# Performance work log

Hardware: AMD Instinct MI355X
Metric: run time of the kernel (lower is better)

The kernel has to match this reference:

```python
import jax, jax.numpy as jnp
import numpy as np

B, S, D, H, DFF = 4, 2048, 2048, 16, 8192
DH = D // H
THETA = 10000.0
EPS = 1e-5


def rmsnorm(x, g):
    return x * jax.lax.rsqrt(jnp.mean(x * x, axis=-1, keepdims=True) + EPS) * g


def rope(x, pos):
    # x: [B, H, S, DH]; rotate interleaved even/odd pairs
    half = DH // 2
    inv_freq = THETA ** (-(jnp.arange(half, dtype=jnp.float32) * 2.0) / DH)  # [half]
    ang = pos.astype(jnp.float32)[:, None] * inv_freq  # [S, half]
    cos, sin = jnp.cos(ang), jnp.sin(ang)
    x1, x2 = x[..., 0::2], x[..., 1::2]
    r1 = x1 * cos - x2 * sin
    r2 = x1 * sin + x2 * cos
    return jnp.stack([r1, r2], axis=-1).reshape(x.shape)


def setup_inputs() -> dict:
    key = jax.random.key(0)
    ks = jax.random.split(key, 12)
    s = 0.02
    return {
        "x": jax.random.normal(ks[0], (B, S, D), dtype=jnp.float32),
        "attention_mask": jnp.ones((S, S), dtype=bool),
        "wq": jax.random.normal(ks[1], (D, D), dtype=jnp.float32) * s,
        "wk": jax.random.normal(ks[2], (D, D), dtype=jnp.float32) * s,
        "wv": jax.random.normal(ks[3], (D, D), dtype=jnp.float32) * s,
        "wo": jax.random.normal(ks[4], (D, D), dtype=jnp.float32) * s,
        "w1": jax.random.normal(ks[5], (DFF, D), dtype=jnp.float32) * s,
        "w2": jax.random.normal(ks[6], (D, DFF), dtype=jnp.float32) * s,
        "w3": jax.random.normal(ks[7], (DFF, D), dtype=jnp.float32) * s,
        "g1": jnp.ones((D,), dtype=jnp.float32),
        "g2": jnp.ones((D,), dtype=jnp.float32),
    }


def reference(x, attention_mask, wq, wk, wv, wo, w1, w2, w3, g1, g2):
    pos = jnp.arange(x.shape[-2])
    # pre-norm attention
    h = rmsnorm(x, g1)
    q = (h @ wq.T).reshape(B, S, H, DH).transpose(0, 2, 1, 3)
    k = (h @ wk.T).reshape(B, S, H, DH).transpose(0, 2, 1, 3)
    v = (h @ wv.T).reshape(B, S, H, DH).transpose(0, 2, 1, 3)
    q = rope(q, pos)
    k = rope(k, pos)
    scores = jnp.einsum("bhqd,bhkd->bhqk", q, k) / np.float32(np.sqrt(DH))
    scores = jnp.where(attention_mask, scores, jnp.float32(-1e9))
    attn = jax.nn.softmax(scores, axis=-1)
    o = jnp.einsum("bhqk,bhkd->bhqd", attn, v)
    o = o.transpose(0, 2, 1, 3).reshape(B, S, D) @ wo.T
    x = x + o
    # pre-norm SwiGLU FFN
    h2 = rmsnorm(x, g2)
    ffn = (jax.nn.silu(h2 @ w1.T) * (h2 @ w3.T)) @ w2.T
    return x + ffn
```

## Files before the change

kernel.cpp:

```cpp
#include <hip/hip_runtime.h>
#include <cstdint>
#include <cstddef>

#define B_   4
#define S_   2048
#define D_   2048
#define H_   16
#define DH_  128
#define DFF_ 8192
#define LOG2E 1.4426950408889634f

typedef __bf16 bf16_t;
typedef __bf16 bf16x4 __attribute__((ext_vector_type(4)));
typedef __bf16 bf16x8 __attribute__((ext_vector_type(8)));
typedef float  f32x4  __attribute__((ext_vector_type(4)));

#define MFMA16 __builtin_amdgcn_mfma_f32_16x16x32_bf16

__device__ __forceinline__ void glds16(const void* g, void* l) {
  __builtin_amdgcn_global_load_lds((__attribute__((address_space(1))) void*)g,
                                   (__attribute__((address_space(3))) void*)l,
                                   16, 0, 0);
}

__global__ __launch_bounds__(256) void cvt_kernel(const float* __restrict__ in,
                                                  bf16_t* __restrict__ out, int n8) {
  int i = blockIdx.x * 256 + threadIdx.x;
  if (i >= n8) return;
  const float4* p4 = (const float4*)in;
  float4 a = p4[2 * (size_t)i];
  float4 b = p4[2 * (size_t)i + 1];
  bf16x8 o;
  o[0] = (bf16_t)a.x; o[1] = (bf16_t)a.y; o[2] = (bf16_t)a.z; o[3] = (bf16_t)a.w;
  o[4] = (bf16_t)b.x; o[5] = (bf16_t)b.y; o[6] = (bf16_t)b.z; o[7] = (bf16_t)b.w;
  ((bf16x8*)out)[i] = o;
}

__global__ __launch_bounds__(256) void rmsnorm_kernel(const float* __restrict__ x,
                                                      const float* __restrict__ g,
                                                      bf16_t* __restrict__ out) {
  const int row = blockIdx.x, tid = threadIdx.x;
  const float* xr = x + (size_t)row * D_;
  float4 a = ((const float4*)xr)[tid * 2];
  float4 b = ((const float4*)xr)[tid * 2 + 1];
  float ss = a.x*a.x + a.y*a.y + a.z*a.z + a.w*a.w
           + b.x*b.x + b.y*b.y + b.z*b.z + b.w*b.w;
#pragma unroll
  for (int m = 1; m < 64; m <<= 1) ss += __shfl_xor(ss, m);
  __shared__ float red[4];
  if ((tid & 63) == 0) red[tid >> 6] = ss;
  __syncthreads();
  float tot = red[0] + red[1] + red[2] + red[3];
  float rms = rsqrtf(tot * (1.0f / D_) + 1e-5f);
  float4 ga = ((const float4*)g)[tid * 2];
  float4 gb = ((const float4*)g)[tid * 2 + 1];
  bf16x8 o;
  o[0] = (bf16_t)(a.x * rms * ga.x); o[1] = (bf16_t)(a.y * rms * ga.y);
  o[2] = (bf16_t)(a.z * rms * ga.z); o[3] = (bf16_t)(a.w * rms * ga.w);
  o[4] = (bf16_t)(b.x * rms * gb.x); o[5] = (bf16_t)(b.y * rms * gb.y);
  o[6] = (bf16_t)(b.z * rms * gb.z); o[7] = (bf16_t)(b.w * rms * gb.w);
  ((bf16x8*)out)[(size_t)row * 256 + tid] = o;
}


#define RD_A_S(d, s)                                                          \
  do {                                                                        \
    const char* p_ = ldsb + (d) * 32768 + ((s) * 64 + l15) * 128;             \
    _Pragma("unroll") for (int i_ = 0; i_ < 4; i_++) {                        \
      afr[i_][0] = *(const bf16x8*)(p_ + i_ * 2048 + acol0);                  \
      afr[i_][1] = *(const bf16x8*)(p_ + i_ * 2048 + acol1);                  \
    }                                                                         \
  } while (0)

#define RD_B(d)                                                               \
  do {                                                                        \
    const char* p_ = ldsb + 65536 + (d) * 32768 + (wn * 32 + l15) * 128;      \
    _Pragma("unroll") for (int j_ = 0; j_ < 2; j_++) {                        \
      bfr[j_][0] = *(const bf16x8*)(p_ + j_ * 2048 + acol0);                  \
      bfr[j_][1] = *(const bf16x8*)(p_ + j_ * 2048 + acol1);                  \
    }                                                                         \
  } while (0)

#define STAGE_A_LO(d, kt)                                                     \
  do {                                                                        \
    char* dst_ = ldsb + (d) * 32768 + o0;                                     \
    const bf16_t* s_ = Asrc + (size_t)(kt) * 64;                              \
    glds16(s_, dst_);                                                         \
    glds16(s_ + 64 * (size_t)K, dst_ + 8192);                                 \
  } while (0)

#define STAGE_A_HI(d, kt)                                                     \
  do {                                                                        \
    char* dst_ = ldsb + (d) * 32768 + 16384 + o0;                             \
    const bf16_t* s_ = Asrc + (size_t)(kt) * 64 + 128 * (size_t)K;            \
    glds16(s_, dst_);                                                         \
    glds16(s_ + 64 * (size_t)K, dst_ + 8192);                                 \
  } while (0)

#define STAGE_B_LO(d, kt)                                                     \
  do {                                                                        \
    char* dst_ = ldsb + 65536 + (d) * 32768 + o0;                             \
    const bf16_t* s_ = Wsrc + (size_t)(kt) * 64;                              \
    glds16(s_, dst_);                                                         \
    glds16(s_ + 64 * (size_t)K, dst_ + 8192);                                 \
  } while (0)

#define STAGE_B_HI(d, kt)                                                     \
  do {                                                                        \
    char* dst_ = ldsb + 65536 + (d) * 32768 + 16384 + o0;                     \
    const bf16_t* s_ = Wsrc + (size_t)(kt) * 64 + 128 * (size_t)K;            \
    glds16(s_, dst_);                                                         \
    glds16(s_ + 64 * (size_t)K, dst_ + 8192);                                 \
  } while (0)

#define MFMA_S(s)                                                             \
  do {                                                                        \
    __builtin_amdgcn_s_setprio(1);                                            \
    _Pragma("unroll") for (int i_ = 0; i_ < 4; i_++)                          \
    _Pragma("unroll") for (int j_ = 0; j_ < 2; j_++) {                        \
      acc[(s)*4 + i_][j_] = MFMA16(afr[i_][0], bfr[j_][0], acc[(s)*4 + i_][j_], 0,0,0); \
      acc[(s)*4 + i_][j_] = MFMA16(afr[i_][1], bfr[j_][1], acc[(s)*4 + i_][j_], 0,0,0); \
    }                                                                         \
    __builtin_amdgcn_s_setprio(0);                                            \
  } while (0)

#define PHASE_FENCE()                                                         \
  do {                                                                        \
    __builtin_amdgcn_sched_barrier(0);                                        \
    __builtin_amdgcn_s_barrier();                                             \
  } while (0)

template <int EPI>
__global__ __launch_bounds__(512, 2) void gemm256(const bf16_t* __restrict__ A,
                                                  const bf16_t* __restrict__ W,
                                                  const float* __restrict__ addf,
                                                  const bf16_t* __restrict__ addb,
                                                  bf16_t* __restrict__ outb,
                                                  bf16_t* __restrict__ outb2,
                                                  bf16_t* __restrict__ outb3,
                                                  float* __restrict__ outf,
                                                  int M, int N, int K) {
  __shared__ char ldsb[131072];
  const int tid = threadIdx.x;
  const int wid = tid >> 6, l = tid & 63, l15 = l & 15, lg = l >> 4;
  const int wn = wid;

  const int nwg = gridDim.x;
  int wg = (int)blockIdx.x;
  wg = (wg & 7) * (nwg >> 3) + (wg >> 3);
  const int ntn = N >> 8;
  const int m0 = (wg / ntn) << 8, n0 = (wg % ntn) << 8;

  f32x4 acc[16][2];
  const f32x4 z4 = {0.f, 0.f, 0.f, 0.f};
#pragma unroll
  for (int i = 0; i < 16; i++) { acc[i][0] = z4; acc[i][1] = z4; }

  const int o0 = tid * 16;
  const int srow = o0 >> 7;
  const int ssw = ((o0 & 127) ^ ((srow & 7) << 4)) >> 1;
  const bf16_t* Asrc = A + (size_t)(m0 + srow) * K + ssw;
  const bf16_t* Wsrc = W + (size_t)(n0 + srow) * K + ssw;

  const int rsw = (l15 & 7) << 4;
  const int acol0 = (lg * 16) ^ rsw;
  const int acol1 = (64 + lg * 16) ^ rsw;

  bf16x8 afr[4][2], bfr[2][2];

  const int NT = K >> 6;
  STAGE_A_LO(0, 0); STAGE_A_HI(0, 0); STAGE_B_LO(0, 0); STAGE_B_HI(0, 0);
  STAGE_B_LO(1, 1); STAGE_A_LO(1, 1); STAGE_B_HI(1, 1);
  asm volatile("s_waitcnt vmcnt(6)" ::: "memory");
  __builtin_amdgcn_s_barrier();

  for (int t = 0; t < NT; t++) {
    const int d = t & 1;
    RD_B(d);
    RD_A_S(d, 0);
    if (t + 1 < NT) STAGE_A_HI(d ^ 1, t + 1);
    PHASE_FENCE();
    MFMA_S(0);
    PHASE_FENCE();
    RD_A_S(d, 1);
    if (t + 2 < NT) STAGE_B_LO(d, t + 2);
    PHASE_FENCE();
    MFMA_S(1);
    PHASE_FENCE();
    RD_A_S(d, 2);
    if (t + 2 < NT) STAGE_A_LO(d, t + 2);
    PHASE_FENCE();
    MFMA_S(2);
    PHASE_FENCE();
    RD_A_S(d, 3);
    if (t + 2 < NT) STAGE_B_HI(d, t + 2);
    PHASE_FENCE();
    MFMA_S(3);
    if (t + 2 < NT) asm volatile("s_waitcnt vmcnt(6)" ::: "memory");
    else            asm volatile("s_waitcnt vmcnt(0)" ::: "memory");
    __builtin_amdgcn_sched_barrier(0);
    __builtin_amdgcn_s_barrier();
  }

#pragma unroll
  for (int m = 0; m < 16; m++) {
    const int gr = m0 + m * 16 + lg * 4;
#pragma unroll
    for (int nn = 0; nn < 2; nn++) {
      const int gc = n0 + wn * 32 + nn * 16 + l15;
      if constexpr (EPI == 4) {
        const int seg = gc >> 11;
        const int gcl = gc & 2047;
        if (seg < 2) {
          bf16_t* o = seg ? outb2 : outb;
#pragma unroll
          for (int r = 0; r < 4; r++)
            o[(size_t)(gr + r) * D_ + gcl] = (bf16_t)acc[m][nn][r];
        } else {
          const int bb = gr >> 11, ss = gr & 2047;
          bf16x4 pk;
#pragma unroll
          for (int r = 0; r < 4; r++) pk[r] = (bf16_t)acc[m][nn][r];
          *(bf16x4*)(outb3 + ((size_t)bb * D_ + gcl) * S_ + ss) = pk;
        }
      } else {
#pragma unroll
        for (int r = 0; r < 4; r++) {
          size_t idx = (size_t)(gr + r) * N + gc;
          if constexpr (EPI == 0) {
            outb[idx] = (bf16_t)acc[m][nn][r];
          } else if constexpr (EPI == 1) {
            outf[idx] = acc[m][nn][r] + addf[idx];
          } else {
            float a1v = (float)addb[idx];
            outb[idx] = (bf16_t)(a1v / (1.0f + expf(-a1v)) * acc[m][nn][r]);
          }
        }
      }
    }
  }
}

__global__ __launch_bounds__(256) void rope_kernel(bf16_t* __restrict__ buf) {
  size_t i = (size_t)blockIdx.x * 256 + threadIdx.x;
  int pi = (int)(i & 63);
  size_t rh = i >> 6;
  int srow = (int)((rh / H_) % S_);
  float inv = expf((float)pi * (-9.210340371976184f / 64.0f));
  float ang = (float)srow * inv;
  float c = cosf(ang), sn = sinf(ang);
  bf16_t* p = buf + i * 2;
  float x1 = (float)p[0], x2 = (float)p[1];
  p[0] = (bf16_t)(x1 * c - x2 * sn);
  p[1] = (bf16_t)(x1 * sn + x2 * c);
}

__global__ __launch_bounds__(256) void attn_kernel(const bf16_t* __restrict__ Q,
                                                   const bf16_t* __restrict__ Kb,
                                                   const bf16_t* __restrict__ Vt,
                                                   bf16_t* __restrict__ O) {
  const int qt = blockIdx.x, h = blockIdx.y, b = blockIdx.z;
  const int tid = threadIdx.x;
  const int wid = tid >> 6, l = tid & 63, l15 = l & 15, lg = l >> 4;

  __shared__ bf16_t Klds[32 * 128];
  __shared__ bf16_t Vlds[128 * 32];
  __shared__ bf16_t Plds[4][16 * 40];

  const int q0 = qt * 64 + wid * 16;
  const f32x4 z4 = {0.f, 0.f, 0.f, 0.f};

  bf16x8 qf[4];
  {
    const bf16_t* qp = Q + ((size_t)(b * S_ + q0 + l15)) * D_ + h * DH_ + lg * 8;
#pragma unroll
    for (int kk = 0; kk < 4; kk++) qf[kk] = *(const bf16x8*)(qp + kk * 32);
  }
  f32x4 of[8];
#pragma unroll
  for (int f = 0; f < 8; f++) of[f] = z4;
  float m_run = -1e30f, l_run = 0.f;

  const int o0 = tid * 16;
  const int krow0 = o0 >> 8;
  const int kcolb = o0 & 255;
  const int scol = (kcolb ^ ((krow0 & 7) << 4)) >> 1;
  const int vrow0 = o0 >> 6;
  const int vc = (o0 >> 4) & 3;
  const int vcol = (vc ^ ((vrow0 >> 1) & 3)) << 3;
  const int vxor = (l15 >> 1) & 3;

  const size_t bh_off = ((size_t)b * S_) * D_ + (size_t)h * DH_;
  const bf16_t* vtbase = Vt + ((size_t)b * D_ + h * DH_) * S_;

  for (int kv0 = 0; kv0 < S_; kv0 += 32) {
    const bf16_t* kbase = Kb + bh_off + (size_t)kv0 * D_;
    glds16(kbase + (size_t)krow0 * D_ + scol,        (char*)Klds + wid * 1024);
    glds16(kbase + (size_t)(krow0 + 16) * D_ + scol, (char*)Klds + wid * 1024 + 4096);
    glds16(vtbase + (size_t)vrow0 * S_ + kv0 + vcol,        (char*)Vlds + wid * 1024);
    glds16(vtbase + (size_t)(vrow0 + 64) * S_ + kv0 + vcol, (char*)Vlds + wid * 1024 + 4096);
    __syncthreads();

    f32x4 st[2];
#pragma unroll
    for (int c = 0; c < 2; c++) {
      st[c] = z4;
      const int row = c * 16 + l15;
      const char* kr = (const char*)Klds + row * 256;
      const int sw = (row & 7) << 4;
#pragma unroll
      for (int kk = 0; kk < 4; kk++) {
        bf16x8 kf = *(const bf16x8*)(kr + ((kk * 64 + lg * 16) ^ sw));
        st[c] = MFMA16(kf, qf[kk], st[c], 0, 0, 0);
      }
    }

    float s[8];
#pragma unroll
    for (int c = 0; c < 2; c++)
#pragma unroll
      for (int r = 0; r < 4; r++) s[c * 4 + r] = st[c][r] * 0.08838834764831845f;
    float pm = s[0];
#pragma unroll
    for (int i = 1; i < 8; i++) pm = fmaxf(pm, s[i]);
    pm = fmaxf(pm, __shfl_xor(pm, 16));
    pm = fmaxf(pm, __shfl_xor(pm, 32));
    float mnew = fmaxf(m_run, pm);
    float alpha = exp2f((m_run - mnew) * LOG2E);
    float p[8], ts = 0.f;
#pragma unroll
    for (int i = 0; i < 8; i++) { p[i] = exp2f((s[i] - mnew) * LOG2E); ts += p[i]; }
    ts += __shfl_xor(ts, 16);
    ts += __shfl_xor(ts, 32);
    l_run = l_run * alpha + ts;
    m_run = mnew;

    float aq[4];
#pragma unroll
    for (int r = 0; r < 4; r++) aq[r] = __shfl(alpha, lg * 4 + r);
#pragma unroll
    for (int f = 0; f < 8; f++)
#pragma unroll
      for (int r = 0; r < 4; r++) of[f][r] *= aq[r];

    bf16_t* pw = &Plds[wid][0];
#pragma unroll
    for (int c = 0; c < 2; c++)
#pragma unroll
      for (int r = 0; r < 4; r++)
        pw[l15 * 40 + c * 16 + lg * 4 + r] = (bf16_t)p[c * 4 + r];
    asm volatile("s_waitcnt lgkmcnt(0)" ::: "memory");
    bf16x8 pa = *(const bf16x8*)(pw + l15 * 40 + lg * 8);
#pragma unroll
    for (int f = 0; f < 8; f++) {
      bf16x8 bv = *(const bf16x8*)((const char*)Vlds + (16 * f + l15) * 64 +
                                   ((lg ^ vxor) << 4));
      of[f] = MFMA16(pa, bv, of[f], 0, 0, 0);
    }
    __syncthreads();
  }

  float inv[4];
#pragma unroll
  for (int r = 0; r < 4; r++) inv[r] = 1.0f / __shfl(l_run, lg * 4 + r);
#pragma unroll
  for (int f = 0; f < 8; f++)
#pragma unroll
    for (int r = 0; r < 4; r++)
      O[((size_t)(b * S_ + q0 + lg * 4 + r)) * D_ + h * DH_ + 16 * f + l15] =
          (bf16_t)(of[f][r] * inv[r]);
}

extern "C" void kernel_launch(void* const* d_in, const int* in_sizes, int n_in,
                              void* d_out, int out_size, void* d_ws, size_t ws_size,
                              hipStream_t stream) {
  const float* x  = (const float*)d_in[0];
  const float* wq = (const float*)d_in[2];
  const float* wk = (const float*)d_in[3];
  const float* wv = (const float*)d_in[4];
  const float* wo = (const float*)d_in[5];
  const float* w1 = (const float*)d_in[6];
  const float* w2 = (const float*)d_in[7];
  const float* w3 = (const float*)d_in[8];
  const float* g1 = (const float*)d_in[9];
  const float* g2 = (const float*)d_in[10];
  float* out = (float*)d_out;

  const size_t ND = (size_t)D_ * D_;
  const size_t NF = (size_t)DFF_ * D_;
  const size_t SLOT = NF * 2;
  char* base = (char*)d_ws;
  bf16_t* wslot = (bf16_t*)(base);
  bf16_t* h1    = (bf16_t*)(base + 1 * SLOT);
  bf16_t* qb    = (bf16_t*)(base + 2 * SLOT);
  bf16_t* kb    = (bf16_t*)(base + 3 * SLOT);
  bf16_t* vt    = (bf16_t*)(base + 4 * SLOT);
  bf16_t* ob    = (bf16_t*)(base + 5 * SLOT);
  bf16_t* h2    = h1;
  bf16_t* g     = qb;
  float*  x1    = out;

  auto cvt = [&](const float* in, bf16_t* o, size_t n) {
    int n8 = (int)(n / 8);
    cvt_kernel<<<(n8 + 255) / 256, 256, 0, stream>>>(in, o, n8);
  };

  rmsnorm_kernel<<<B_ * S_, 256, 0, stream>>>(x, g1, h1);

  cvt(wq, wslot, ND);
  cvt(wk, wslot + ND, ND);
  cvt(wv, wslot + 2 * ND, ND);
  const int gqkv3 = (8192 / 256) * (6144 / 256);
  gemm256<4><<<gqkv3, 512, 0, stream>>>(h1, wslot, nullptr, nullptr,
                                        qb, kb, vt, nullptr, 8192, 6144, 2048);

  rope_kernel<<<(B_ * S_ * H_ * 64) / 256, 256, 0, stream>>>(qb);
  rope_kernel<<<(B_ * S_ * H_ * 64) / 256, 256, 0, stream>>>(kb);

  dim3 ga(S_ / 64, H_, B_);
  attn_kernel<<<ga, 256, 0, stream>>>(qb, kb, vt, ob);

  const int gqkv = (8192 / 256) * (2048 / 256);
  cvt(wo, wslot, ND);
  gemm256<1><<<gqkv, 512, 0, stream>>>(ob, wslot, x, nullptr,
                                       nullptr, nullptr, nullptr, x1, 8192, 2048, 2048);

  rmsnorm_kernel<<<B_ * S_, 256, 0, stream>>>(x1, g2, h2);

  const int gff = (8192 / 256) * (8192 / 256);
  cvt(w1, wslot, NF);
  gemm256<0><<<gff, 512, 0, stream>>>(h2, wslot, nullptr, nullptr,
                                      g, nullptr, nullptr, nullptr, 8192, 8192, 2048);

  cvt(w3, wslot, NF);
  gemm256<2><<<gff, 512, 0, stream>>>(h2, wslot, nullptr, g,
                                      g, nullptr, nullptr, nullptr, 8192, 8192, 2048);

  cvt(w2, wslot, NF);
  gemm256<1><<<gqkv, 512, 0, stream>>>(g, wslot, x1, nullptr,
                                       nullptr, nullptr, nullptr, x1, 8192, 2048, 8192);
}
```

Baseline: 1.528 ms.

## Add register double-buffered GEMM variant for the FFN w1/w3 projections

```diff
diff --git a/kernel.cpp b/kernel.cpp
--- a/kernel.cpp
+++ b/kernel.cpp
@@ -63,25 +63,31 @@
 }
 
 
-#define RD_A_S(d, s)                                                          \
+#define RDA(dst, d, s)                                                        \
   do {                                                                        \
     const char* p_ = ldsb + (d) * 32768 + ((s) * 64 + l15) * 128;             \
     _Pragma("unroll") for (int i_ = 0; i_ < 4; i_++) {                        \
-      afr[i_][0] = *(const bf16x8*)(p_ + i_ * 2048 + acol0);                  \
-      afr[i_][1] = *(const bf16x8*)(p_ + i_ * 2048 + acol1);                  \
+      dst[i_][0] = *(const bf16x8*)(p_ + i_ * 2048 + acol0);                  \
+      dst[i_][1] = *(const bf16x8*)(p_ + i_ * 2048 + acol1);                  \
     }                                                                         \
   } while (0)
 
-#define RD_B(d)                                                               \
+#define RDB(dst, d)                                                           \
   do {                                                                        \
     const char* p_ = ldsb + 65536 + (d) * 32768 + (wn * 32 + l15) * 128;      \
     _Pragma("unroll") for (int j_ = 0; j_ < 2; j_++) {                        \
-      bfr[j_][0] = *(const bf16x8*)(p_ + j_ * 2048 + acol0);                  \
-      bfr[j_][1] = *(const bf16x8*)(p_ + j_ * 2048 + acol1);                  \
+      dst[j_][0] = *(const bf16x8*)(p_ + j_ * 2048 + acol0);                  \
+      dst[j_][1] = *(const bf16x8*)(p_ + j_ * 2048 + acol1);                  \
     }                                                                         \
   } while (0)
 
-#define STAGE_A_LO(d, kt)                                                     \
+#define RDAB(dstA, da, s, dstB, db)                                           \
+  do {                                                                        \
+    RDA(dstA, da, s);                                                         \
+    RDB(dstB, db);                                                            \
+  } while (0)
+
+#define STG_AL(d, kt)                                                         \
   do {                                                                        \
     char* dst_ = ldsb + (d) * 32768 + o0;                                     \
     const bf16_t* s_ = Asrc + (size_t)(kt) * 64;                              \
@@ -89,7 +95,7 @@
     glds16(s_ + 64 * (size_t)K, dst_ + 8192);                                 \
   } while (0)
 
-#define STAGE_A_HI(d, kt)                                                     \
+#define STG_AH(d, kt)                                                         \
   do {                                                                        \
     char* dst_ = ldsb + (d) * 32768 + 16384 + o0;                             \
     const bf16_t* s_ = Asrc + (size_t)(kt) * 64 + 128 * (size_t)K;            \
@@ -97,7 +103,7 @@
     glds16(s_ + 64 * (size_t)K, dst_ + 8192);                                 \
   } while (0)
 
-#define STAGE_B_LO(d, kt)                                                     \
+#define STG_BL(d, kt)                                                         \
   do {                                                                        \
     char* dst_ = ldsb + 65536 + (d) * 32768 + o0;                             \
     const bf16_t* s_ = Wsrc + (size_t)(kt) * 64;                              \
@@ -105,7 +111,7 @@
     glds16(s_ + 64 * (size_t)K, dst_ + 8192);                                 \
   } while (0)
 
-#define STAGE_B_HI(d, kt)                                                     \
+#define STG_BH(d, kt)                                                         \
   do {                                                                        \
     char* dst_ = ldsb + 65536 + (d) * 32768 + 16384 + o0;                     \
     const bf16_t* s_ = Wsrc + (size_t)(kt) * 64 + 128 * (size_t)K;            \
@@ -113,22 +119,63 @@
     glds16(s_ + 64 * (size_t)K, dst_ + 8192);                                 \
   } while (0)
 
-#define MFMA_S(s)                                                             \
+#define MFMA_SP(s, Aset, Bset)                                                \
   do {                                                                        \
     __builtin_amdgcn_s_setprio(1);                                            \
     _Pragma("unroll") for (int i_ = 0; i_ < 4; i_++)                          \
     _Pragma("unroll") for (int j_ = 0; j_ < 2; j_++) {                        \
-      acc[(s)*4 + i_][j_] = MFMA16(afr[i_][0], bfr[j_][0], acc[(s)*4 + i_][j_], 0,0,0); \
-      acc[(s)*4 + i_][j_] = MFMA16(afr[i_][1], bfr[j_][1], acc[(s)*4 + i_][j_], 0,0,0); \
+      acc[(s)*4 + i_][j_] = MFMA16(Aset[i_][0], Bset[j_][0], acc[(s)*4 + i_][j_], 0,0,0); \
+      acc[(s)*4 + i_][j_] = MFMA16(Aset[i_][1], Bset[j_][1], acc[(s)*4 + i_][j_], 0,0,0); \
     }                                                                         \
     __builtin_amdgcn_s_setprio(0);                                            \
   } while (0)
 
-#define PHASE_FENCE()                                                         \
+#define VM2()  asm volatile("s_waitcnt vmcnt(2)" ::: "memory")
+#define MIDFENCE()                                                            \
   do {                                                                        \
     __builtin_amdgcn_sched_barrier(0);                                        \
     __builtin_amdgcn_s_barrier();                                             \
-  } while (0)
+    __builtin_amdgcn_sched_barrier(0);                                        \
+  } while (0)
+#define ENDFENCE()                                                            \
+  do {                                                                        \
+    __builtin_amdgcn_sched_barrier(0);                                        \
+    __builtin_amdgcn_s_barrier();                                             \
+  } while (0)
+
+#define GEMM_EPILOGUE()                                                       \
+  _Pragma("unroll") for (int m = 0; m < 16; m++) {                            \
+    const int gr = m0 + m * 16 + lg * 4;                                      \
+    _Pragma("unroll") for (int nn = 0; nn < 2; nn++) {                        \
+      const int gc = n0 + wn * 32 + nn * 16 + l15;                            \
+      if constexpr (EPI == 4) {                                               \
+        const int seg = gc >> 11;                                             \
+        const int gcl = gc & 2047;                                            \
+        if (seg < 2) {                                                        \
+          bf16_t* o = seg ? outb2 : outb;                                     \
+          _Pragma("unroll") for (int r = 0; r < 4; r++)                       \
+            o[(size_t)(gr + r) * D_ + gcl] = (bf16_t)acc[m][nn][r];           \
+        } else {                                                              \
+          const int bb = gr >> 11, ss = gr & 2047;                            \
+          bf16x4 pk;                                                          \
+          _Pragma("unroll") for (int r = 0; r < 4; r++) pk[r] = (bf16_t)acc[m][nn][r]; \
+          *(bf16x4*)(outb3 + ((size_t)bb * D_ + gcl) * S_ + ss) = pk;         \
+        }                                                                     \
+      } else {                                                                \
+        _Pragma("unroll") for (int r = 0; r < 4; r++) {                       \
+          size_t idx = (size_t)(gr + r) * N + gc;                             \
+          if constexpr (EPI == 0) {                                           \
+            outb[idx] = (bf16_t)acc[m][nn][r];                                \
+          } else if constexpr (EPI == 1) {                                    \
+            outf[idx] = acc[m][nn][r] + addf[idx];                            \
+          } else {                                                            \
+            float a1v = (float)addb[idx];                                     \
+            outb[idx] = (bf16_t)(a1v / (1.0f + expf(-a1v)) * acc[m][nn][r]);  \
+          }                                                                   \
+        }                                                                     \
+      }                                                                       \
+    }                                                                         \
+  }
 
 template <int EPI>
 __global__ __launch_bounds__(512, 2) void gemm256(const bf16_t* __restrict__ A,
@@ -169,76 +216,118 @@
   bf16x8 afr[4][2], bfr[2][2];
 
   const int NT = K >> 6;
-  STAGE_A_LO(0, 0); STAGE_A_HI(0, 0); STAGE_B_LO(0, 0); STAGE_B_HI(0, 0);
-  STAGE_B_LO(1, 1); STAGE_A_LO(1, 1); STAGE_B_HI(1, 1);
+  STG_AL(0, 0); STG_AH(0, 0); STG_BL(0, 0); STG_BH(0, 0);
+  STG_BL(1, 1); STG_AL(1, 1); STG_BH(1, 1);
   asm volatile("s_waitcnt vmcnt(6)" ::: "memory");
   __builtin_amdgcn_s_barrier();
 
   for (int t = 0; t < NT; t++) {
     const int d = t & 1;
-    RD_B(d);
-    RD_A_S(d, 0);
-    if (t + 1 < NT) STAGE_A_HI(d ^ 1, t + 1);
-    PHASE_FENCE();
-    MFMA_S(0);
-    PHASE_FENCE();
-    RD_A_S(d, 1);
-    if (t + 2 < NT) STAGE_B_LO(d, t + 2);
-    PHASE_FENCE();
-    MFMA_S(1);
-    PHASE_FENCE();
-    RD_A_S(d, 2);
-    if (t + 2 < NT) STAGE_A_LO(d, t + 2);
-    PHASE_FENCE();
-    MFMA_S(2);
-    PHASE_FENCE();
-    RD_A_S(d, 3);
-    if (t + 2 < NT) STAGE_B_HI(d, t + 2);
-    PHASE_FENCE();
-    MFMA_S(3);
+    RDB(bfr, d);
+    RDA(afr, d, 0);
+    if (t + 1 < NT) STG_AH(d ^ 1, t + 1);
+    MIDFENCE();
+    MFMA_SP(0, afr, bfr);
+    ENDFENCE();
+    RDA(afr, d, 1);
+    if (t + 2 < NT) STG_BL(d, t + 2);
+    MIDFENCE();
+    MFMA_SP(1, afr, bfr);
+    ENDFENCE();
+    RDA(afr, d, 2);
+    if (t + 2 < NT) STG_AL(d, t + 2);
+    MIDFENCE();
+    MFMA_SP(2, afr, bfr);
+    ENDFENCE();
+    RDA(afr, d, 3);
+    if (t + 2 < NT) STG_BH(d, t + 2);
+    MIDFENCE();
+    MFMA_SP(3, afr, bfr);
     if (t + 2 < NT) asm volatile("s_waitcnt vmcnt(6)" ::: "memory");
     else            asm volatile("s_waitcnt vmcnt(0)" ::: "memory");
     __builtin_amdgcn_sched_barrier(0);
     __builtin_amdgcn_s_barrier();
   }
 
-#pragma unroll
-  for (int m = 0; m < 16; m++) {
-    const int gr = m0 + m * 16 + lg * 4;
-#pragma unroll
-    for (int nn = 0; nn < 2; nn++) {
-      const int gc = n0 + wn * 32 + nn * 16 + l15;
-      if constexpr (EPI == 4) {
-        const int seg = gc >> 11;
-        const int gcl = gc & 2047;
-        if (seg < 2) {
-          bf16_t* o = seg ? outb2 : outb;
-#pragma unroll
-          for (int r = 0; r < 4; r++)
-            o[(size_t)(gr + r) * D_ + gcl] = (bf16_t)acc[m][nn][r];
-        } else {
-          const int bb = gr >> 11, ss = gr & 2047;
-          bf16x4 pk;
-#pragma unroll
-          for (int r = 0; r < 4; r++) pk[r] = (bf16_t)acc[m][nn][r];
-          *(bf16x4*)(outb3 + ((size_t)bb * D_ + gcl) * S_ + ss) = pk;
-        }
-      } else {
-#pragma unroll
-        for (int r = 0; r < 4; r++) {
-          size_t idx = (size_t)(gr + r) * N + gc;
-          if constexpr (EPI == 0) {
-            outb[idx] = (bf16_t)acc[m][nn][r];
-          } else if constexpr (EPI == 1) {
-            outf[idx] = acc[m][nn][r] + addf[idx];
-          } else {
-            float a1v = (float)addb[idx];
-            outb[idx] = (bf16_t)(a1v / (1.0f + expf(-a1v)) * acc[m][nn][r]);
-          }
-        }
-      }
-    }
+  GEMM_EPILOGUE()
+}
+
+template <int EPI>
+__global__ __launch_bounds__(512, 2) void gemm256p(const bf16_t* __restrict__ A,
+                                                   const bf16_t* __restrict__ W,
+                                                   const float* __restrict__ addf,
+                                                   const bf16_t* __restrict__ addb,
+                                                   bf16_t* __restrict__ outb,
+                                                   bf16_t* __restrict__ outb2,
+                                                   bf16_t* __restrict__ outb3,
+                                                   float* __restrict__ outf,
+                                                   int M, int N, int K) {
+  __shared__ char ldsb[131072];
+  const int tid = threadIdx.x;
+  const int wid = tid >> 6, l = tid & 63, l15 = l & 15, lg = l >> 4;
+  const int wn = wid;
+
+  const int nwg = gridDim.x;
+  int wg = (int)blockIdx.x;
+  wg = (wg & 7) * (nwg >> 3) + (wg >> 3);
+  const int ntn = N >> 8;
+  const int m0 = (wg / ntn) << 8, n0 = (wg % ntn) << 8;
+
+  f32x4 acc[16][2];
+  const f32x4 z4 = {0.f, 0.f, 0.f, 0.f};
+#pragma unroll
+  for (int i = 0; i < 16; i++) { acc[i][0] = z4; acc[i][1] = z4; }
+
+  const int o0 = tid * 16;
+  const int srow = o0 >> 7;
+  const int ssw = ((o0 & 127) ^ ((srow & 7) << 4)) >> 1;
+  const bf16_t* Asrc = A + (size_t)(m0 + srow) * K + ssw;
+  const bf16_t* Wsrc = W + (size_t)(n0 + srow) * K + ssw;
+
+  const int rsw = (l15 & 7) << 4;
+  const int acol0 = (lg * 16) ^ rsw;
+  const int acol1 = (64 + lg * 16) ^ rsw;
+
+  bf16x8 aX[4][2], aY[4][2], bA[2][2], bB[2][2];
+
+  const int NT = K >> 6;
+
+  STG_AL(0, 0); STG_AH(0, 0); STG_BL(0, 0); STG_BH(0, 0);
+  asm volatile("s_waitcnt vmcnt(0)" ::: "memory");
+  __builtin_amdgcn_s_barrier();
+  RDA(aX, 0, 0);
+  RDB(bA, 0);
+  STG_AL(1, 1);
+  STG_BL(1, 1);
+
+#define PIPE_PHASE(s, Acur, Bcur, RD_NEXT, STG_STMT)                          \
+  do {                                                                        \
+    VM2();                                                                    \
+    RD_NEXT;                                                                  \
+    STG_STMT;                                                                 \
+    MIDFENCE();                                                               \
+    MFMA_SP(s, Acur, Bcur);                                                   \
+    ENDFENCE();                                                               \
+  } while (0)
+
+  for (int t = 0; t < NT; t += 2) {
+    PIPE_PHASE(0, aX, bA, RDA(aY, 0, 1), STG_BH(1, t + 1));
+    PIPE_PHASE(1, aY, bA, RDA(aX, 0, 2), STG_AH(1, t + 1));
+    PIPE_PHASE(2, aX, bA, RDA(aY, 0, 3),
+               if (t + 2 < NT) STG_AL(0, t + 2));
+    PIPE_PHASE(3, aY, bA, RDAB(aX, 1, 0, bB, 1),
+               if (t + 2 < NT) STG_BL(0, t + 2));
+    PIPE_PHASE(0, aX, bB, RDA(aY, 1, 1),
+               if (t + 2 < NT) STG_BH(0, t + 2));
+    PIPE_PHASE(1, aY, bB, RDA(aX, 1, 2),
+               if (t + 2 < NT) STG_AH(0, t + 2));
+    PIPE_PHASE(2, aX, bB, RDA(aY, 1, 3),
+               if (t + 3 < NT) STG_AL(1, t + 3));
+    PIPE_PHASE(3, aY, bB, RDAB(aX, 0, 0, bA, 0),
+               if (t + 3 < NT) STG_BL(1, t + 3));
   }
+
+  GEMM_EPILOGUE()
 }
 
 __global__ __launch_bounds__(256) void rope_kernel(bf16_t* __restrict__ buf) {
@@ -429,12 +518,12 @@
 
   const int gff = (8192 / 256) * (8192 / 256);
   cvt(w1, wslot, NF);
-  gemm256<0><<<gff, 512, 0, stream>>>(h2, wslot, nullptr, nullptr,
-                                      g, nullptr, nullptr, nullptr, 8192, 8192, 2048);
+  gemm256p<0><<<gff, 512, 0, stream>>>(h2, wslot, nullptr, nullptr,
+                                       g, nullptr, nullptr, nullptr, 8192, 8192, 2048);
 
   cvt(w3, wslot, NF);
-  gemm256<2><<<gff, 512, 0, stream>>>(h2, wslot, nullptr, g,
-                                      g, nullptr, nullptr, nullptr, 8192, 8192, 2048);
+  gemm256p<2><<<gff, 512, 0, stream>>>(h2, wslot, nullptr, g,
+                                       g, nullptr, nullptr, nullptr, 8192, 8192, 2048);
 
   cvt(w2, wslot, NF);
   gemm256<1><<<gqkv, 512, 0, stream>>>(g, wslot, x1, nullptr,
```

Measured after the change: 2.172 ms. 42.1% more time.
